# Optimization experiments

Measured on AMD Instinct MI355X. Metric: run time of the kernel, lower is better.

Reference implementation:

```python
import jax, jax.numpy as jnp
import numpy as np

B, S, T = 1024, 512, 48


def setup_inputs() -> dict:
    key = jax.random.key(0)
    k1, k2, k3, k4, k5 = jax.random.split(key, 5)
    feats = jax.random.normal(k1, (B, S, T), dtype=jnp.float32)
    tags = jax.random.randint(k2, (B, S), 0, T)
    mask = jnp.ones((B, S), dtype=bool)
    transitions = jax.random.normal(k3, (T, T), dtype=jnp.float32)
    start_transitions = jax.random.normal(k4, (T,), dtype=jnp.float32)
    stop_transitions = jax.random.normal(k5, (T,), dtype=jnp.float32)
    return dict(feats=feats, tags=tags, mask=mask, transitions=transitions,
                start_transitions=start_transitions, stop_transitions=stop_transitions)


def _crf_nll(feats, transitions, start_transitions, stop_transitions, tags, mask):
    # ----- forward algorithm (log partition) -----
    fv0 = start_transitions + feats[:, 0]                      # (B, T)

    def step(fv, xs):
        feat_t, mask_t = xs                                    # (B, T), (B,)
        # transitions[next, cur]: fv over cur axis (last)
        nxt = jax.nn.logsumexp(fv[:, None, :] + transitions[None, :, :]
                               + feat_t[:, :, None], axis=-1)  # (B, T)
        fv = jnp.where(mask_t[:, None], nxt, fv)
        return fv, None

    feats_t = jnp.swapaxes(feats, 0, 1)                        # (S, B, T)
    fv, _ = jax.lax.scan(step, fv0, (feats_t[1:], mask.T[1:]))
    log_z = jax.nn.logsumexp(fv + stop_transitions, axis=-1)   # (B,)

    # ----- gold path score -----
    emit = jnp.take_along_axis(feats, tags[..., None], axis=2)[..., 0]   # (B, S)
    trans = transitions[tags[:, 1:], tags[:, :-1]]                       # (B, S-1)
    gold = emit[:, 0] + start_transitions[tags[:, 0]]
    gold = gold + jnp.sum(jnp.where(mask[:, 1:], trans + emit[:, 1:], 0.0), axis=1)
    last_idx = mask.astype(jnp.int32).sum(axis=1) - 1                    # (B,)
    last_tag = jnp.take_along_axis(tags, last_idx[:, None], axis=1)[:, 0]
    gold = gold + stop_transitions[last_tag]

    return jnp.mean(log_z - gold)


def reference(feats, tags, mask, transitions, start_transitions, stop_transitions):
    return _crf_nll(feats, transitions, start_transitions, stop_transitions, tags, mask)
```

## Files before the change

kernel.cpp:

```cpp
#include <hip/hip_runtime.h>
#include <hip/hip_bf16.h>
#include <math.h>

#define BB 1024
#define SS 512
#define MID 256
#define TT 48
#define BPW 16
#define FWG 64
#define BWG 64

typedef __attribute__((ext_vector_type(8))) short short8;
typedef __attribute__((ext_vector_type(4))) float f32x4;
typedef __attribute__((ext_vector_type(4))) unsigned u32x4;
typedef __attribute__((ext_vector_type(2))) unsigned u32x2;

__device__ __forceinline__ unsigned short f2bf_u(float x) {
    return __builtin_bit_cast(unsigned short, __float2bfloat16(x));
}
__device__ __forceinline__ unsigned pk_bf16(float lo, float hi) {
    return (unsigned)f2bf_u(lo) | ((unsigned)f2bf_u(hi) << 16);
}
__device__ __forceinline__ short f2bf(float x) { return (short)f2bf_u(x); }

template<int CTRL>
__device__ __forceinline__ float dpp_f(float v) {
    int r = __builtin_amdgcn_update_dpp(0, __builtin_bit_cast(int, v),
                                        CTRL, 0xF, 0xF, true);
    return __builtin_bit_cast(float, r);
}
__device__ __forceinline__ float waveSum(float v) {
    v += dpp_f<0x111>(v);
    v += dpp_f<0x112>(v);
    v += dpp_f<0x114>(v);
    v += dpp_f<0x118>(v);
    v += dpp_f<0x142>(v);
    v += dpp_f<0x143>(v);
    return __builtin_bit_cast(float,
        __builtin_amdgcn_readlane(__builtin_bit_cast(int, v), 63));
}

__global__ __launch_bounds__(64, 1) void crf_main(
    const float* __restrict__ feats, const int* __restrict__ tags,
    const float* __restrict__ trans, const float* __restrict__ startT,
    const float* __restrict__ stopT,
    float* __restrict__ qf, float* __restrict__ cf,
    float* __restrict__ qb, float* __restrict__ cb,
    float* __restrict__ gold)
{
    const int lane = threadIdx.x;

    if (blockIdx.x < FWG + BWG) {
        const bool isF = blockIdx.x < FWG;
        __shared__ unsigned Q[16][28];
        __shared__ int ptab[16];
        const int c = lane & 15;
        const int g = lane >> 4;
        const int bi = isF ? blockIdx.x : (blockIdx.x - FWG);
        const int b0 = bi * BPW;
        const float* fb = feats + (size_t)(b0 + c) * SS * TT;

        int pic;
        {
            if (lane < 16) ptab[lane] = lane;
            const short one = f2bf(1.0f);
            short8 PA, PB;
            #pragma unroll
            for (int j = 0; j < 8; j++) {
                PA[j] = (g == 0) ? one : (short)0;
                PB[j] = f2bf((float)c);
            }
            f32x4 z = {0.f, 0.f, 0.f, 0.f};
            f32x4 PD = __builtin_amdgcn_mfma_f32_16x16x32_bf16(PA, PB, z, 0, 0, 0);
            int piv = (int)(PD[0] * 0.125f + 0.5f);
            piv = piv < 0 ? 0 : (piv > 15 ? 15 : piv);
            if (g == 0) ptab[piv] = c;
            pic = ptab[c];
            pic = pic < 0 ? 0 : (pic > 15 ? 15 : pic);
        }

        short8 Afr[3][2];
        #pragma unroll
        for (int r = 0; r < 3; r++)
            #pragma unroll
            for (int s = 0; s < 2; s++) {
                short8 v;
                #pragma unroll
                for (int j = 0; j < 8; j++) {
                    int k = 8 * g + j + 32 * s;
                    int row = 16 * r + c;
                    float e = (k < TT)
                        ? __expf(isF ? trans[row * TT + k] : trans[k * TT + row])
                        : 0.0f;
                    v[j] = f2bf(e);
                }
                Afr[r][s] = v;
            }

        f32x4 prods[3];
        float c_acc = 0.0f;
        float pend_is = 1.0f, pend_lg = 0.0f;
        f32x4 rA[3], rB[3], rC[3], Ecur[3];

        #define PUBLISH_READ() do {                                          \
            _Pragma("unroll")                                                \
            for (int r = 0; r < 3; r++) {                                    \
                u32x2 w = { pk_bf16(prods[r][0], prods[r][1]),               \
                            pk_bf16(prods[r][2], prods[r][3]) };             \
                *(u32x2*)(&Q[c][8 * r + 2 * g]) = w;                         \
            }                                                                \
            const unsigned* src = &Q[pic][0];                                \
            B0 = __builtin_bit_cast(short8, *(const u32x4*)(src + 4 * g));   \
            if (g < 2)                                                       \
                B1 = __builtin_bit_cast(short8, *(const u32x4*)(src + 16 + 4 * g)); \
            else { u32x4 zz = {0u,0u,0u,0u}; B1 = __builtin_bit_cast(short8, zz); } \
        } while (0)

        #define MEASURE() do {                                               \
            float mx = 0.0f;                                                 \
            _Pragma("unroll")                                                \
            for (int r = 0; r < 3; r++)                                      \
                _Pragma("unroll")                                            \
                for (int j = 0; j < 4; j++) {                                \
                    prods[r][j] = fminf(prods[r][j], 1e30f);                 \
                    mx = fmaxf(mx, prods[r][j]);                             \
                }                                                            \
            mx = fmaxf(mx, __shfl_xor(mx, 16));                              \
            mx = fmaxf(mx, __shfl_xor(mx, 32));                              \
            mx = fminf(fmaxf(mx, 1e-30f), 3e37f);                            \
            pend_is = __builtin_amdgcn_rcpf(mx);                             \
            pend_lg = __logf(mx);                                            \
        } while (0)

        #define FOLD() do {                                                  \
            c_acc += pend_lg;                                                \
            _Pragma("unroll")                                                \
            for (int r = 0; r < 3; r++) Ecur[r] *= pend_is;                  \
        } while (0)

        short8 B0, B1;

        if (isF) {
            {
                f32x4 fv[3];
                #pragma unroll
                for (int r = 0; r < 3; r++) {
                    f32x4 st = *(const f32x4*)(startT + 16 * r + 4 * g);
                    f32x4 f0 = *(const f32x4*)(fb + 16 * r + 4 * g);
                    fv[r] = st + f0;
                }
                float mx = fv[0][0];
                #pragma unroll
                for (int r = 0; r < 3; r++)
                    #pragma unroll
                    for (int j = 0; j < 4; j++) mx = fmaxf(mx, fv[r][j]);
                mx = fmaxf(mx, __shfl_xor(mx, 16));
                mx = fmaxf(mx, __shfl_xor(mx, 32));
                c_acc = mx;
                #pragma unroll
                for (int r = 0; r < 3; r++)
                    #pragma unroll
                    for (int j = 0; j < 4; j++)
                        prods[r][j] = __expf(fv[r][j] - mx);
            }
            PUBLISH_READ();
            #pragma unroll
            for (int r = 0; r < 3; r++) {
                f32x4 r1 = *(const f32x4*)(fb + (size_t)1 * TT + 16 * r + 4 * g);
                rA[r] = *(const f32x4*)(fb + (size_t)2 * TT + 16 * r + 4 * g);
                rB[r] = *(const f32x4*)(fb + (size_t)3 * TT + 16 * r + 4 * g);
                rC[r] = *(const f32x4*)(fb + (size_t)4 * TT + 16 * r + 4 * g);
                f32x4 e;
                #pragma unroll
                for (int j = 0; j < 4; j++) e[j] = __expf(r1[j]);
                Ecur[r] = e;
            }

            #pragma unroll 4
            for (int t = 1; t <= MID; t++) {
                int tl = (t + 4 <= MID) ? t + 4 : MID;
                f32x4 rN[3];
                #pragma unroll
                for (int r = 0; r < 3; r++)
                    rN[r] = *(const f32x4*)(fb + (size_t)tl * TT + 16 * r + 4 * g);

                f32x4 D[3];
                #pragma unroll
                for (int r = 0; r < 3; r++) {
                    f32x4 z = {0.f, 0.f, 0.f, 0.f};
                    z = __builtin_amdgcn_mfma_f32_16x16x32_bf16(Afr[r][0], B0, z, 0, 0, 0);
                    z = __builtin_amdgcn_mfma_f32_16x16x32_bf16(Afr[r][1], B1, z, 0, 0, 0);
                    D[r] = z;
                }
                if ((t & 3) == 1) FOLD();
                #pragma unroll
                for (int r = 0; r < 3; r++) prods[r] = D[r] * Ecur[r];
                if ((t & 3) == 0) MEASURE();
                PUBLISH_READ();
                #pragma unroll
                for (int r = 0; r < 3; r++) {
                    f32x4 e;
                    #pragma unroll
                    for (int j = 0; j < 4; j++) e[j] = __expf(rA[r][j]);
                    Ecur[r] = e;
                    rA[r] = rB[r];
                    rB[r] = rC[r];
                    rC[r] = rN[r];
                }
            }
            #pragma unroll
            for (int r = 0; r < 3; r++)
                *(f32x4*)(qf + (size_t)(b0 + c) * TT + 16 * r + 4 * g) = prods[r];
            if (g == 0) cf[b0 + c] = c_acc;
        } else {
            #pragma unroll
            for (int r = 0; r < 3; r++) {
                f32x4 sp = *(const f32x4*)(stopT + 16 * r + 4 * g);
                #pragma unroll
                for (int j = 0; j < 4; j++) prods[r][j] = __expf(sp[j]);
            }
            #pragma unroll
            for (int r = 0; r < 3; r++) {
                f32x4 r1 = *(const f32x4*)(fb + (size_t)(SS - 1) * TT + 16 * r + 4 * g);
                rA[r] = *(const f32x4*)(fb + (size_t)(SS - 2) * TT + 16 * r + 4 * g);
                rB[r] = *(const f32x4*)(fb + (size_t)(SS - 3) * TT + 16 * r + 4 * g);
                rC[r] = *(const f32x4*)(fb + (size_t)(SS - 4) * TT + 16 * r + 4 * g);
                f32x4 e;
                #pragma unroll
                for (int j = 0; j < 4; j++) e[j] = __expf(r1[j]);
                Ecur[r] = e;
            }

            #pragma unroll 4
            for (int t = SS - 1; t >= MID + 1; t--) {
                int tl = (t - 4 >= 0) ? t - 4 : 0;
                f32x4 rN[3];
                #pragma unroll
                for (int r = 0; r < 3; r++)
                    rN[r] = *(const f32x4*)(fb + (size_t)tl * TT + 16 * r + 4 * g);

                if ((t & 3) == 3) FOLD();
                #pragma unroll
                for (int r = 0; r < 3; r++) prods[r] = prods[r] * Ecur[r];
                PUBLISH_READ();
                f32x4 D[3];
                #pragma unroll
                for (int r = 0; r < 3; r++) {
                    f32x4 z = {0.f, 0.f, 0.f, 0.f};
                    z = __builtin_amdgcn_mfma_f32_16x16x32_bf16(Afr[r][0], B0, z, 0, 0, 0);
                    z = __builtin_amdgcn_mfma_f32_16x16x32_bf16(Afr[r][1], B1, z, 0, 0, 0);
                    D[r] = z;
                }
                #pragma unroll
                for (int r = 0; r < 3; r++) prods[r] = D[r];
                if ((t & 3) == 0) MEASURE();
                #pragma unroll
                for (int r = 0; r < 3; r++) {
                    f32x4 e;
                    #pragma unroll
                    for (int j = 0; j < 4; j++) e[j] = __expf(rA[r][j]);
                    Ecur[r] = e;
                    rA[r] = rB[r];
                    rB[r] = rC[r];
                    rC[r] = rN[r];
                }
            }
            #pragma unroll
            for (int r = 0; r < 3; r++)
                *(f32x4*)(qb + (size_t)(b0 + c) * TT + 16 * r + 4 * g) = prods[r];
            if (g == 0) cb[b0 + c] = c_acc;
        }
        #undef PUBLISH_READ
        #undef MEASURE
        #undef FOLD
    } else {
        const int b = blockIdx.x - FWG - BWG;
        const int* tg = tags + b * SS;
        const float* fbg = feats + (size_t)b * SS * TT;
        float acc = 0.0f;
        for (int t = lane; t < SS; t += 64) {
            int cur = tg[t];
            if (t == 0) {
                acc += fbg[cur] + startT[cur];
            } else {
                int prev = tg[t - 1];
                acc += fbg[t * TT + cur] + trans[cur * TT + prev];
            }
        }
        float tot = waveSum(acc);
        if (lane == 0) gold[b] = tot + stopT[tg[SS - 1]];
    }
}

__global__ __launch_bounds__(256) void crf_final(
    const float* __restrict__ qf, const float* __restrict__ cf,
    const float* __restrict__ qb, const float* __restrict__ cb,
    const float* __restrict__ gold, float* __restrict__ out)
{
    __shared__ double sh[256];
    int t = threadIdx.x;
    double s = 0.0;
    for (int b = t * 4; b < t * 4 + 4; b++) {
        float acc = 0.0f;
        for (int j = 0; j < TT; j++)
            acc += qf[(size_t)b * TT + j] * qb[(size_t)b * TT + j];
        acc = fminf(fmaxf(acc, 1e-35f), 3e37f);
        float lz = cf[b] + cb[b] + __logf(acc);
        s += (double)lz - (double)gold[b];
    }
    sh[t] = s;
    __syncthreads();
    for (int ofs = 128; ofs > 0; ofs >>= 1) {
        if (t < ofs) sh[t] += sh[t + ofs];
        __syncthreads();
    }
    if (t == 0) out[0] = (float)(sh[0] / (double)BB);
}

extern "C" void kernel_launch(void* const* d_in, const int* in_sizes, int n_in,
                              void* d_out, int out_size, void* d_ws, size_t ws_size,
                              hipStream_t stream)
{
    const float* feats  = (const float*)d_in[0];
    const int*   tags   = (const int*)d_in[1];
    const float* trans  = (const float*)d_in[3];
    const float* startT = (const float*)d_in[4];
    const float* stopT  = (const float*)d_in[5];

    float* gold = (float*)d_ws;
    float* qf   = gold + BB;
    float* cf   = qf + BB * TT;
    float* qb   = cf + BB;
    float* cb   = qb + BB * TT;

    crf_main<<<FWG + BWG + BB, 64, 0, stream>>>(
        feats, tags, trans, startT, stopT, qf, cf, qb, cb, gold);
    crf_final<<<1, 256, 0, stream>>>(qf, cf, qb, cb, gold, (float*)d_out);
}
```

Baseline: 124.1 us.

## Split sequence into three segments with a parallel middle transfer-matrix pass

The sequential chain is split into three segments: a forward pass over the first third, a backward pass over the last third, and a middle segment computed as a 48x48 transfer matrix. Each middle column runs in its own workgroup (3 per batch of 16 columns), and the results are joined in a new combine kernel. This shortens the critical serial path from about 256 steps to about 170 and uses many more workgroups. The cost is a large amount of extra middle work (48 columns per sequence), bf16 storage of the transfer matrix, and an additional kernel launch.

```diff
diff --git a/kernel.cpp b/kernel.cpp
--- a/kernel.cpp
+++ b/kernel.cpp
@@ -4,11 +4,14 @@
 
 #define BB 1024
 #define SS 512
-#define MID 256
 #define TT 48
-#define BPW 16
-#define FWG 64
-#define BWG 64
+#define SEG_A 170
+#define SEG_B 341
+#define NFWD 64
+#define NBWD 64
+#define NMID 3072
+#define MIDBASE 128
+#define GOLDBASE 3200
 
 typedef __attribute__((ext_vector_type(8))) short short8;
 typedef __attribute__((ext_vector_type(4))) float f32x4;
@@ -46,235 +49,13 @@
     const float* __restrict__ stopT,
     float* __restrict__ qf, float* __restrict__ cf,
     float* __restrict__ qb, float* __restrict__ cb,
+    float* __restrict__ cM, unsigned* __restrict__ Mw,
     float* __restrict__ gold)
 {
     const int lane = threadIdx.x;
 
-    if (blockIdx.x < FWG + BWG) {
-        const bool isF = blockIdx.x < FWG;
-        __shared__ unsigned Q[16][28];
-        __shared__ int ptab[16];
-        const int c = lane & 15;
-        const int g = lane >> 4;
-        const int bi = isF ? blockIdx.x : (blockIdx.x - FWG);
-        const int b0 = bi * BPW;
-        const float* fb = feats + (size_t)(b0 + c) * SS * TT;
-
-        int pic;
-        {
-            if (lane < 16) ptab[lane] = lane;
-            const short one = f2bf(1.0f);
-            short8 PA, PB;
-            #pragma unroll
-            for (int j = 0; j < 8; j++) {
-                PA[j] = (g == 0) ? one : (short)0;
-                PB[j] = f2bf((float)c);
-            }
-            f32x4 z = {0.f, 0.f, 0.f, 0.f};
-            f32x4 PD = __builtin_amdgcn_mfma_f32_16x16x32_bf16(PA, PB, z, 0, 0, 0);
-            int piv = (int)(PD[0] * 0.125f + 0.5f);
-            piv = piv < 0 ? 0 : (piv > 15 ? 15 : piv);
-            if (g == 0) ptab[piv] = c;
-            pic = ptab[c];
-            pic = pic < 0 ? 0 : (pic > 15 ? 15 : pic);
-        }
-
-        short8 Afr[3][2];
-        #pragma unroll
-        for (int r = 0; r < 3; r++)
-            #pragma unroll
-            for (int s = 0; s < 2; s++) {
-                short8 v;
-                #pragma unroll
-                for (int j = 0; j < 8; j++) {
-                    int k = 8 * g + j + 32 * s;
-                    int row = 16 * r + c;
-                    float e = (k < TT)
-                        ? __expf(isF ? trans[row * TT + k] : trans[k * TT + row])
-                        : 0.0f;
-                    v[j] = f2bf(e);
-                }
-                Afr[r][s] = v;
-            }
-
-        f32x4 prods[3];
-        float c_acc = 0.0f;
-        float pend_is = 1.0f, pend_lg = 0.0f;
-        f32x4 rA[3], rB[3], rC[3], Ecur[3];
-
-        #define PUBLISH_READ() do {                                          \
-            _Pragma("unroll")                                                \
-            for (int r = 0; r < 3; r++) {                                    \
-                u32x2 w = { pk_bf16(prods[r][0], prods[r][1]),               \
-                            pk_bf16(prods[r][2], prods[r][3]) };             \
-                *(u32x2*)(&Q[c][8 * r + 2 * g]) = w;                         \
-            }                                                                \
-            const unsigned* src = &Q[pic][0];                                \
-            B0 = __builtin_bit_cast(short8, *(const u32x4*)(src + 4 * g));   \
-            if (g < 2)                                                       \
-                B1 = __builtin_bit_cast(short8, *(const u32x4*)(src + 16 + 4 * g)); \
-            else { u32x4 zz = {0u,0u,0u,0u}; B1 = __builtin_bit_cast(short8, zz); } \
-        } while (0)
-
-        #define MEASURE() do {                                               \
-            float mx = 0.0f;                                                 \
-            _Pragma("unroll")                                                \
-            for (int r = 0; r < 3; r++)                                      \
-                _Pragma("unroll")                                            \
-                for (int j = 0; j < 4; j++) {                                \
-                    prods[r][j] = fminf(prods[r][j], 1e30f);                 \
-                    mx = fmaxf(mx, prods[r][j]);                             \
-                }                                                            \
-            mx = fmaxf(mx, __shfl_xor(mx, 16));                              \
-            mx = fmaxf(mx, __shfl_xor(mx, 32));                              \
-            mx = fminf(fmaxf(mx, 1e-30f), 3e37f);                            \
-            pend_is = __builtin_amdgcn_rcpf(mx);                             \
-            pend_lg = __logf(mx);                                            \
-        } while (0)
-
-        #define FOLD() do {                                                  \
-            c_acc += pend_lg;                                                \
-            _Pragma("unroll")                                                \
-            for (int r = 0; r < 3; r++) Ecur[r] *= pend_is;                  \
-        } while (0)
-
-        short8 B0, B1;
-
-        if (isF) {
-            {
-                f32x4 fv[3];
-                #pragma unroll
-                for (int r = 0; r < 3; r++) {
-                    f32x4 st = *(const f32x4*)(startT + 16 * r + 4 * g);
-                    f32x4 f0 = *(const f32x4*)(fb + 16 * r + 4 * g);
-                    fv[r] = st + f0;
-                }
-                float mx = fv[0][0];
-                #pragma unroll
-                for (int r = 0; r < 3; r++)
-                    #pragma unroll
-                    for (int j = 0; j < 4; j++) mx = fmaxf(mx, fv[r][j]);
-                mx = fmaxf(mx, __shfl_xor(mx, 16));
-                mx = fmaxf(mx, __shfl_xor(mx, 32));
-                c_acc = mx;
-                #pragma unroll
-                for (int r = 0; r < 3; r++)
-                    #pragma unroll
-                    for (int j = 0; j < 4; j++)
-                        prods[r][j] = __expf(fv[r][j] - mx);
-            }
-            PUBLISH_READ();
-            #pragma unroll
-            for (int r = 0; r < 3; r++) {
-                f32x4 r1 = *(const f32x4*)(fb + (size_t)1 * TT + 16 * r + 4 * g);
-                rA[r] = *(const f32x4*)(fb + (size_t)2 * TT + 16 * r + 4 * g);
-                rB[r] = *(const f32x4*)(fb + (size_t)3 * TT + 16 * r + 4 * g);
-                rC[r] = *(const f32x4*)(fb + (size_t)4 * TT + 16 * r + 4 * g);
-                f32x4 e;
-                #pragma unroll
-                for (int j = 0; j < 4; j++) e[j] = __expf(r1[j]);
-                Ecur[r] = e;
-            }
-
-            #pragma unroll 4
-            for (int t = 1; t <= MID; t++) {
-                int tl = (t + 4 <= MID) ? t + 4 : MID;
-                f32x4 rN[3];
-                #pragma unroll
-                for (int r = 0; r < 3; r++)
-                    rN[r] = *(const f32x4*)(fb + (size_t)tl * TT + 16 * r + 4 * g);
-
-                f32x4 D[3];
-                #pragma unroll
-                for (int r = 0; r < 3; r++) {
-                    f32x4 z = {0.f, 0.f, 0.f, 0.f};
-                    z = __builtin_amdgcn_mfma_f32_16x16x32_bf16(Afr[r][0], B0, z, 0, 0, 0);
-                    z = __builtin_amdgcn_mfma_f32_16x16x32_bf16(Afr[r][1], B1, z, 0, 0, 0);
-                    D[r] = z;
-                }
-                if ((t & 3) == 1) FOLD();
-                #pragma unroll
-                for (int r = 0; r < 3; r++) prods[r] = D[r] * Ecur[r];
-                if ((t & 3) == 0) MEASURE();
-                PUBLISH_READ();
-                #pragma unroll
-                for (int r = 0; r < 3; r++) {
-                    f32x4 e;
-                    #pragma unroll
-                    for (int j = 0; j < 4; j++) e[j] = __expf(rA[r][j]);
-                    Ecur[r] = e;
-                    rA[r] = rB[r];
-                    rB[r] = rC[r];
-                    rC[r] = rN[r];
-                }
-            }
-            #pragma unroll
-            for (int r = 0; r < 3; r++)
-                *(f32x4*)(qf + (size_t)(b0 + c) * TT + 16 * r + 4 * g) = prods[r];
-            if (g == 0) cf[b0 + c] = c_acc;
-        } else {
-            #pragma unroll
-            for (int r = 0; r < 3; r++) {
-                f32x4 sp = *(const f32x4*)(stopT + 16 * r + 4 * g);
-                #pragma unroll
-                for (int j = 0; j < 4; j++) prods[r][j] = __expf(sp[j]);
-            }
-            #pragma unroll
-            for (int r = 0; r < 3; r++) {
-                f32x4 r1 = *(const f32x4*)(fb + (size_t)(SS - 1) * TT + 16 * r + 4 * g);
-                rA[r] = *(const f32x4*)(fb + (size_t)(SS - 2) * TT + 16 * r + 4 * g);
-                rB[r] = *(const f32x4*)(fb + (size_t)(SS - 3) * TT + 16 * r + 4 * g);
-                rC[r] = *(const f32x4*)(fb + (size_t)(SS - 4) * TT + 16 * r + 4 * g);
-                f32x4 e;
-                #pragma unroll
-                for (int j = 0; j < 4; j++) e[j] = __expf(r1[j]);
-                Ecur[r] = e;
-            }
-
-            #pragma unroll 4
-            for (int t = SS - 1; t >= MID + 1; t--) {
-                int tl = (t - 4 >= 0) ? t - 4 : 0;
-                f32x4 rN[3];
-                #pragma unroll
-                for (int r = 0; r < 3; r++)
-                    rN[r] = *(const f32x4*)(fb + (size_t)tl * TT + 16 * r + 4 * g);
-
-                if ((t & 3) == 3) FOLD();
-                #pragma unroll
-                for (int r = 0; r < 3; r++) prods[r] = prods[r] * Ecur[r];
-                PUBLISH_READ();
-                f32x4 D[3];
-                #pragma unroll
-                for (int r = 0; r < 3; r++) {
-                    f32x4 z = {0.f, 0.f, 0.f, 0.f};
-                    z = __builtin_amdgcn_mfma_f32_16x16x32_bf16(Afr[r][0], B0, z, 0, 0, 0);
-                    z = __builtin_amdgcn_mfma_f32_16x16x32_bf16(Afr[r][1], B1, z, 0, 0, 0);
-                    D[r] = z;
-                }
-                #pragma unroll
-                for (int r = 0; r < 3; r++) prods[r] = D[r];
-                if ((t & 3) == 0) MEASURE();
-                #pragma unroll
-                for (int r = 0; r < 3; r++) {
-                    f32x4 e;
-                    #pragma unroll
-                    for (int j = 0; j < 4; j++) e[j] = __expf(rA[r][j]);
-                    Ecur[r] = e;
-                    rA[r] = rB[r];
-                    rB[r] = rC[r];
-                    rC[r] = rN[r];
-                }
-            }
-            #pragma unroll
-            for (int r = 0; r < 3; r++)
-                *(f32x4*)(qb + (size_t)(b0 + c) * TT + 16 * r + 4 * g) = prods[r];
-            if (g == 0) cb[b0 + c] = c_acc;
-        }
-        #undef PUBLISH_READ
-        #undef MEASURE
-        #undef FOLD
-    } else {
-        const int b = blockIdx.x - FWG - BWG;
+    if (blockIdx.x >= GOLDBASE) {
+        const int b = blockIdx.x - GOLDBASE;
         const int* tg = tags + b * SS;
         const float* fbg = feats + (size_t)b * SS * TT;
         float acc = 0.0f;
@@ -289,25 +70,334 @@
         }
         float tot = waveSum(acc);
         if (lane == 0) gold[b] = tot + stopT[tg[SS - 1]];
-    }
-}
-
-__global__ __launch_bounds__(256) void crf_final(
+        return;
+    }
+
+    const int role = blockIdx.x < NFWD ? 0 : (blockIdx.x < MIDBASE ? 1 : 2);
+    const bool isBwd = (role == 1);
+
+    __shared__ unsigned Q[16][28];
+    __shared__ int ptab[16];
+    const int c = lane & 15;
+    const int g = lane >> 4;
+
+    int b0 = 0, batch = 0, colID = 0;
+    size_t fbIdx;
+    if (role == 2) {
+        int m = blockIdx.x - MIDBASE;
+        batch = m / 3;
+        colID = (m - batch * 3) * 16 + c;
+        fbIdx = (size_t)batch;
+    } else {
+        int bi = isBwd ? (blockIdx.x - NFWD) : blockIdx.x;
+        b0 = bi * 16;
+        fbIdx = (size_t)(b0 + c);
+    }
+    const float* fb = feats + fbIdx * (size_t)(SS * TT);
+
+    int pic;
+    {
+        if (lane < 16) ptab[lane] = lane;
+        const short one = f2bf(1.0f);
+        short8 PA, PB;
+        #pragma unroll
+        for (int j = 0; j < 8; j++) {
+            PA[j] = (g == 0) ? one : (short)0;
+            PB[j] = f2bf((float)c);
+        }
+        f32x4 z = {0.f, 0.f, 0.f, 0.f};
+        f32x4 PD = __builtin_amdgcn_mfma_f32_16x16x32_bf16(PA, PB, z, 0, 0, 0);
+        int piv = (int)(PD[0] * 0.125f + 0.5f);
+        piv = piv < 0 ? 0 : (piv > 15 ? 15 : piv);
+        if (g == 0) ptab[piv] = c;
+        pic = ptab[c];
+        pic = pic < 0 ? 0 : (pic > 15 ? 15 : pic);
+    }
+
+    short8 Afr[3][2];
+    #pragma unroll
+    for (int r = 0; r < 3; r++)
+        #pragma unroll
+        for (int s = 0; s < 2; s++) {
+            short8 v;
+            #pragma unroll
+            for (int j = 0; j < 8; j++) {
+                int k = 8 * g + j + 32 * s;
+                int row = 16 * r + c;
+                float e = (k < TT)
+                    ? __expf(isBwd ? trans[k * TT + row] : trans[row * TT + k])
+                    : 0.0f;
+                v[j] = f2bf(e);
+            }
+            Afr[r][s] = v;
+        }
+
+    f32x4 prods[3];
+    float c_acc = 0.0f;
+    float pend_is = 1.0f, pend_lg = 0.0f;
+    f32x4 rA[3], rB[3], rC[3], Ecur[3];
+    short8 B0, B1;
+
+    #define PUBLISH_READ() do {                                          \
+        _Pragma("unroll")                                                \
+        for (int r = 0; r < 3; r++) {                                    \
+            u32x2 w = { pk_bf16(prods[r][0], prods[r][1]),               \
+                        pk_bf16(prods[r][2], prods[r][3]) };             \
+            *(u32x2*)(&Q[c][8 * r + 2 * g]) = w;                         \
+        }                                                                \
+        const unsigned* src = &Q[pic][0];                                \
+        B0 = __builtin_bit_cast(short8, *(const u32x4*)(src + 4 * g));   \
+        if (g < 2)                                                       \
+            B1 = __builtin_bit_cast(short8, *(const u32x4*)(src + 16 + 4 * g)); \
+        else { u32x4 zz = {0u,0u,0u,0u}; B1 = __builtin_bit_cast(short8, zz); } \
+    } while (0)
+
+    #define MEASURE() do {                                               \
+        float mx = 0.0f;                                                 \
+        _Pragma("unroll")                                                \
+        for (int r = 0; r < 3; r++)                                      \
+            _Pragma("unroll")                                            \
+            for (int j = 0; j < 4; j++) {                                \
+                prods[r][j] = fminf(prods[r][j], 1e30f);                 \
+                mx = fmaxf(mx, prods[r][j]);                             \
+            }                                                            \
+        mx = fmaxf(mx, __shfl_xor(mx, 16));                              \
+        mx = fmaxf(mx, __shfl_xor(mx, 32));                              \
+        mx = fminf(fmaxf(mx, 1e-30f), 3e37f);                            \
+        pend_is = __builtin_amdgcn_rcpf(mx);                             \
+        pend_lg = __logf(mx);                                            \
+    } while (0)
+
+    #define FOLD() do {                                                  \
+        c_acc += pend_lg;                                                \
+        _Pragma("unroll")                                                \
+        for (int r = 0; r < 3; r++) Ecur[r] *= pend_is;                  \
+    } while (0)
+
+    #define FINAL_NORM() do {                                            \
+        float mx = 0.0f;                                                 \
+        _Pragma("unroll")                                                \
+        for (int r = 0; r < 3; r++)                                      \
+            _Pragma("unroll")                                            \
+            for (int j = 0; j < 4; j++) {                                \
+                prods[r][j] = fminf(prods[r][j], 1e30f);                 \
+                mx = fmaxf(mx, prods[r][j]);                             \
+            }                                                            \
+        mx = fmaxf(mx, __shfl_xor(mx, 16));                              \
+        mx = fmaxf(mx, __shfl_xor(mx, 32));                              \
+        mx = fminf(fmaxf(mx, 1e-30f), 3e37f);                            \
+        c_acc += __logf(mx);                                             \
+        float inv = __builtin_amdgcn_rcpf(mx);                           \
+        _Pragma("unroll")                                                \
+        for (int r = 0; r < 3; r++) prods[r] *= inv;                     \
+    } while (0)
+
+    #define FWD_PREFETCH(T0) do {                                        \
+        _Pragma("unroll")                                                \
+        for (int r = 0; r < 3; r++) {                                    \
+            f32x4 r1 = *(const f32x4*)(fb + (size_t)(T0) * TT + 16 * r + 4 * g);       \
+            rA[r] = *(const f32x4*)(fb + (size_t)((T0) + 1) * TT + 16 * r + 4 * g);    \
+            rB[r] = *(const f32x4*)(fb + (size_t)((T0) + 2) * TT + 16 * r + 4 * g);    \
+            rC[r] = *(const f32x4*)(fb + (size_t)((T0) + 3) * TT + 16 * r + 4 * g);    \
+            f32x4 e;                                                     \
+            _Pragma("unroll")                                            \
+            for (int j = 0; j < 4; j++) e[j] = __expf(r1[j]);            \
+            Ecur[r] = e;                                                 \
+        }                                                                \
+    } while (0)
+
+    #define FWD_LOOP(T0, T1)                                             \
+        _Pragma("unroll 4")                                              \
+        for (int t = (T0); t <= (T1); t++) {                             \
+            int tl = (t + 4 <= (T1)) ? t + 4 : (T1);                     \
+            f32x4 rN[3];                                                 \
+            _Pragma("unroll")                                            \
+            for (int r = 0; r < 3; r++)                                  \
+                rN[r] = *(const f32x4*)(fb + (size_t)tl * TT + 16 * r + 4 * g); \
+            f32x4 D[3];                                                  \
+            _Pragma("unroll")                                            \
+            for (int r = 0; r < 3; r++) {                                \
+                f32x4 z = {0.f, 0.f, 0.f, 0.f};                          \
+                z = __builtin_amdgcn_mfma_f32_16x16x32_bf16(Afr[r][0], B0, z, 0, 0, 0); \
+                z = __builtin_amdgcn_mfma_f32_16x16x32_bf16(Afr[r][1], B1, z, 0, 0, 0); \
+                D[r] = z;                                                \
+            }                                                            \
+            if ((t & 3) == 1) FOLD();                                    \
+            _Pragma("unroll")                                            \
+            for (int r = 0; r < 3; r++) prods[r] = D[r] * Ecur[r];       \
+            if ((t & 3) == 0) MEASURE();                                 \
+            PUBLISH_READ();                                              \
+            _Pragma("unroll")                                            \
+            for (int r = 0; r < 3; r++) {                                \
+                f32x4 e;                                                 \
+                _Pragma("unroll")                                        \
+                for (int j = 0; j < 4; j++) e[j] = __expf(rA[r][j]);     \
+                Ecur[r] = e;                                             \
+                rA[r] = rB[r]; rB[r] = rC[r]; rC[r] = rN[r];             \
+            }                                                            \
+        }
+
+    if (role == 0) {
+        {
+            f32x4 fv[3];
+            #pragma unroll
+            for (int r = 0; r < 3; r++) {
+                f32x4 st = *(const f32x4*)(startT + 16 * r + 4 * g);
+                f32x4 f0 = *(const f32x4*)(fb + 16 * r + 4 * g);
+                fv[r] = st + f0;
+            }
+            float mx = fv[0][0];
+            #pragma unroll
+            for (int r = 0; r < 3; r++)
+                #pragma unroll
+                for (int j = 0; j < 4; j++) mx = fmaxf(mx, fv[r][j]);
+            mx = fmaxf(mx, __shfl_xor(mx, 16));
+            mx = fmaxf(mx, __shfl_xor(mx, 32));
+            c_acc = mx;
+            #pragma unroll
+            for (int r = 0; r < 3; r++)
+                #pragma unroll
+                for (int j = 0; j < 4; j++)
+                    prods[r][j] = __expf(fv[r][j] - mx);
+        }
+        PUBLISH_READ();
+        FWD_PREFETCH(1);
+        FWD_LOOP(1, SEG_A)
+        FINAL_NORM();
+        #pragma unroll
+        for (int r = 0; r < 3; r++)
+            *(f32x4*)(qf + (size_t)(b0 + c) * TT + 16 * r + 4 * g) = prods[r];
+        if (g == 0) cf[b0 + c] = c_acc;
+    } else if (role == 2) {
+        #pragma unroll
+        for (int r = 0; r < 3; r++)
+            #pragma unroll
+            for (int j = 0; j < 4; j++)
+                prods[r][j] = (16 * r + 4 * g + j == colID) ? 1.0f : 0.0f;
+        PUBLISH_READ();
+        FWD_PREFETCH(SEG_A + 1);
+        FWD_LOOP(SEG_A + 1, SEG_B)
+        FINAL_NORM();
+        unsigned* Mb = Mw + ((size_t)batch * TT + colID) * 24;
+        #pragma unroll
+        for (int r = 0; r < 3; r++) {
+            Mb[8 * r + 2 * g + 0] = pk_bf16(prods[r][0], prods[r][1]);
+            Mb[8 * r + 2 * g + 1] = pk_bf16(prods[r][2], prods[r][3]);
+        }
+        if (g == 0) cM[batch * TT + colID] = c_acc;
+    } else {
+        #pragma unroll
+        for (int r = 0; r < 3; r++) {
+            f32x4 sp = *(const f32x4*)(stopT + 16 * r + 4 * g);
+            #pragma unroll
+            for (int j = 0; j < 4; j++) prods[r][j] = __expf(sp[j]);
+        }
+        #pragma unroll
+        for (int r = 0; r < 3; r++) {
+            f32x4 r1 = *(const f32x4*)(fb + (size_t)(SS - 1) * TT + 16 * r + 4 * g);
+            rA[r] = *(const f32x4*)(fb + (size_t)(SS - 2) * TT + 16 * r + 4 * g);
+            rB[r] = *(const f32x4*)(fb + (size_t)(SS - 3) * TT + 16 * r + 4 * g);
+            rC[r] = *(const f32x4*)(fb + (size_t)(SS - 4) * TT + 16 * r + 4 * g);
+            f32x4 e;
+            #pragma unroll
+            for (int j = 0; j < 4; j++) e[j] = __expf(r1[j]);
+            Ecur[r] = e;
+        }
+        #pragma unroll 4
+        for (int t = SS - 1; t >= SEG_B + 1; t--) {
+            int tl = (t - 4 >= 0) ? t - 4 : 0;
+            f32x4 rN[3];
+            #pragma unroll
+            for (int r = 0; r < 3; r++)
+                rN[r] = *(const f32x4*)(fb + (size_t)tl * TT + 16 * r + 4 * g);
+            if ((t & 3) == 3) FOLD();
+            #pragma unroll
+            for (int r = 0; r < 3; r++) prods[r] = prods[r] * Ecur[r];
+            PUBLISH_READ();
+            f32x4 D[3];
+            #pragma unroll
+            for (int r = 0; r < 3; r++) {
+                f32x4 z = {0.f, 0.f, 0.f, 0.f};
+                z = __builtin_amdgcn_mfma_f32_16x16x32_bf16(Afr[r][0], B0, z, 0, 0, 0);
+                z = __builtin_amdgcn_mfma_f32_16x16x32_bf16(Afr[r][1], B1, z, 0, 0, 0);
+                D[r] = z;
+            }
+            #pragma unroll
+            for (int r = 0; r < 3; r++) prods[r] = D[r];
+            if ((t & 3) == 0) MEASURE();
+            #pragma unroll
+            for (int r = 0; r < 3; r++) {
+                f32x4 e;
+                #pragma unroll
+                for (int j = 0; j < 4; j++) e[j] = __expf(rA[r][j]);
+                Ecur[r] = e;
+                rA[r] = rB[r]; rB[r] = rC[r]; rC[r] = rN[r];
+            }
+        }
+        FINAL_NORM();
+        #pragma unroll
+        for (int r = 0; r < 3; r++)
+            *(f32x4*)(qb + (size_t)(b0 + c) * TT + 16 * r + 4 * g) = prods[r];
+        if (g == 0) cb[b0 + c] = c_acc;
+    }
+    #undef PUBLISH_READ
+    #undef MEASURE
+    #undef FOLD
+    #undef FINAL_NORM
+    #undef FWD_PREFETCH
+    #undef FWD_LOOP
+}
+
+__global__ __launch_bounds__(256) void crf_combine(
     const float* __restrict__ qf, const float* __restrict__ cf,
     const float* __restrict__ qb, const float* __restrict__ cb,
-    const float* __restrict__ gold, float* __restrict__ out)
+    const float* __restrict__ cM, const unsigned* __restrict__ Mw,
+    const float* __restrict__ gold, float* __restrict__ nll)
+{
+    __shared__ float tsh[4][64];
+    const int wv = threadIdx.x >> 6;
+    const int lane = threadIdx.x & 63;
+    const int b = blockIdx.x * 4 + wv;
+    const bool a = lane < TT;
+    const int lc = a ? lane : (TT - 1);
+
+    float qfv = a ? qf[(size_t)b * TT + lane] : 0.0f;
+    float cMv = a ? cM[(size_t)b * TT + lane] : -3e38f;
+    float qbv = a ? qb[(size_t)b * TT + lane] : 0.0f;
+
+    float cmax = cMv;
+    #pragma unroll
+    for (int d = 1; d < 64; d <<= 1)
+        cmax = fmaxf(cmax, __shfl_xor(cmax, d));
+
+    float tv = a ? qfv * __expf(cMv - cmax) : 0.0f;
+    tsh[wv][lane] = tv;
+
+    const unsigned* Mb = Mw + (size_t)b * TT * 24;
+    float w = 0.0f;
+    for (int j = 0; j < TT; j++) {
+        unsigned word = Mb[j * 24 + (lc >> 1)];
+        unsigned bits = (lc & 1) ? (word & 0xffff0000u) : (word << 16);
+        w += __builtin_bit_cast(float, bits) * tsh[wv][j];
+    }
+    float s = a ? qbv * w : 0.0f;
+    s += __shfl_xor(s, 1);  s += __shfl_xor(s, 2);
+    s += __shfl_xor(s, 4);  s += __shfl_xor(s, 8);
+    s += __shfl_xor(s, 16); s += __shfl_xor(s, 32);
+    if (lane == 0) {
+        s = fminf(fmaxf(s, 1e-35f), 3e37f);
+        float lz = cf[b] + cb[b] + cmax + __logf(s);
+        nll[b] = lz - gold[b];
+    }
+}
+
+__global__ __launch_bounds__(256) void crf_mean(
+    const float* __restrict__ nll, float* __restrict__ out)
 {
     __shared__ double sh[256];
     int t = threadIdx.x;
     double s = 0.0;
-    for (int b = t * 4; b < t * 4 + 4; b++) {
-        float acc = 0.0f;
-        for (int j = 0; j < TT; j++)
-            acc += qf[(size_t)b * TT + j] * qb[(size_t)b * TT + j];
-        acc = fminf(fmaxf(acc, 1e-35f), 3e37f);
-        float lz = cf[b] + cb[b] + __logf(acc);
-        s += (double)lz - (double)gold[b];
-    }
+    for (int k = t; k < BB; k += 256) s += (double)nll[k];
     sh[t] = s;
     __syncthreads();
     for (int ofs = 128; ofs > 0; ofs >>= 1) {
@@ -327,13 +417,17 @@
     const float* startT = (const float*)d_in[4];
     const float* stopT  = (const float*)d_in[5];
 
-    float* gold = (float*)d_ws;
-    float* qf   = gold + BB;
-    float* cf   = qf + BB * TT;
-    float* qb   = cf + BB;
-    float* cb   = qb + BB * TT;
-
-    crf_main<<<FWG + BWG + BB, 64, 0, stream>>>(
-        feats, tags, trans, startT, stopT, qf, cf, qb, cb, gold);
-    crf_final<<<1, 256, 0, stream>>>(qf, cf, qb, cb, gold, (float*)d_out);
-}
+    float*    gold = (float*)d_ws;
+    float*    qf   = gold + BB;
+    float*    cf   = qf + BB * TT;
+    float*    qb   = cf + BB;
+    float*    cb   = qb + BB * TT;
+    float*    cM   = cb + BB;
+    unsigned* Mw   = (unsigned*)(cM + BB * TT);
+    float*    nll  = (float*)(Mw + (size_t)BB * TT * 24);
+
+    crf_main<<<GOLDBASE + BB, 64, 0, stream>>>(
+        feats, tags, trans, startT, stopT, qf, cf, qb, cb, cM, Mw, gold);
+    crf_combine<<<BB / 4, 256, 0, stream>>>(qf, cf, qb, cb, cM, Mw, gold, nll);
+    crf_mean<<<1, 256, 0, stream>>>(nll, (float*)d_out);
+}
```

Measured after the change: 170.3 us. 1.37x slower.
